# Performance work log

Measured on AMD Instinct MI355X. Metric: run time of the kernel, lower is better.

Reference implementation:

```python
import jax, jax.numpy as jnp
import numpy as np

# RankPool1d config (from init_kwargs)
RANK = 8          # kth smallest (1-indexed, as in torch.kthvalue)
KERNEL_SIZE = 16
STRIDE = 1
PADDING = 8
PAD_VALUE = 0.0   # mode='constant'

L = 4_194_304


def setup_inputs() -> dict:
    key = jax.random.key(0)
    x = jax.random.normal(key, (L,), dtype=jnp.float32)
    return {"x": x}


def reference(x):
    # F.pad(input, (PADDING, PADDING), mode='constant', value=PAD_VALUE)
    p = jnp.pad(x, (PADDING, PADDING), mode="constant", constant_values=PAD_VALUE)
    # p.unfold(0, KERNEL_SIZE, STRIDE) -> [out_len, KERNEL_SIZE] overlapping windows
    out_len = (p.shape[0] - KERNEL_SIZE) // STRIDE + 1
    idx = jnp.arange(out_len)[:, None] * STRIDE + jnp.arange(KERNEL_SIZE)[None, :]
    windows = p[idx]  # [out_len, k]
    # kthvalue(k=RANK, dim=1): value and index (within window) of RANK-th smallest
    order = jnp.argsort(windows, axis=1)          # [out_len, k]
    sel = order[:, RANK - 1]                       # [out_len] window-local index
    values = jnp.take_along_axis(windows, sel[:, None], axis=1)[:, 0]  # [out_len]
    return values, sel.astype(jnp.int32)
```

## Files before the change

### kernel.cpp

```cpp
#include <hip/hip_runtime.h>


constexpr int L_IN    = 4194304;
constexpr int OUT_LEN = L_IN + 1;
constexpr int MOUT    = 16;
constexpr int TPB     = 256;
constexpr int OPB     = TPB * MOUT;

__global__ __launch_bounds__(TPB) void rankpool_kernel(const float* __restrict__ x,
                                                       float* __restrict__ dout) {
    __shared__ float lv[MOUT * TPB];
    __shared__ float ls[MOUT * TPB];

    const int t   = threadIdx.x;
    const int blk = blockIdx.x;

    if (blk == 1024) {
        if (t == 0) {
            float w[16];
            #pragma unroll
            for (int i = 0; i < 16; ++i) {
                int g = L_IN - 8 + i;
                w[i] = (g < L_IN) ? x[g] : 0.0f;
            }
            int R[16];
            #pragma unroll
            for (int j = 0; j < 16; ++j) R[j] = j;
            #pragma unroll
            for (int j = 0; j < 16; ++j)
                #pragma unroll
                for (int k = j + 1; k < 16; ++k) {
                    int c = (w[k] < w[j]);
                    R[j] += c; R[k] -= c;
                }
            int sel = 0; float val = w[0];
            #pragma unroll
            for (int j = 0; j < 16; ++j) {
                bool c = (R[j] == 7);
                sel = c ? j : sel; val = c ? w[j] : val;
            }
            dout[OUT_LEN - 1]     = val;
            dout[2 * OUT_LEN - 1] = (float)sel;
        }
        return;
    }

    const int o0   = (blk * TPB + t) * MOUT;
    const int base = o0 - 8;

    float w[32];
    if (base >= 0 && base + 32 <= L_IN) {
        const float4* p = reinterpret_cast<const float4*>(x + base);
        #pragma unroll
        for (int q = 0; q < 8; ++q) {
            float4 v = p[q];
            w[4*q+0] = v.x; w[4*q+1] = v.y; w[4*q+2] = v.z; w[4*q+3] = v.w;
        }
    } else {
        #pragma unroll
        for (int i = 0; i < 32; ++i) {
            int g = base + i;
            w[i] = (g >= 0 && g < L_IN) ? x[g] : 0.0f;
        }
    }

    int R[31];
    #pragma unroll
    for (int j = 0; j < 16; ++j) R[j] = j;
    #pragma unroll
    for (int j = 0; j < 16; ++j) {
        #pragma unroll
        for (int k = j + 1; k < 16; ++k) {
            int c = (w[k] < w[j]);
            R[j] += c;
            R[k] -= c;
        }
    }

    #pragma unroll
    for (int m = 0; m < MOUT; ++m) {
        int   sel = 0;
        float val = w[m];
        #pragma unroll
        for (int j = m; j < m + 16; ++j) {
            bool c = (R[j] == 7 + m);
            sel = c ? (j - m) : sel;
            val = c ? w[j]    : val;
        }
        lv[m * TPB + t] = val;
        ls[m * TPB + t] = (float)sel;

        if (m < MOUT - 1) {
            const float wm = w[m];
            const float wn = w[m + 16];
            int s = 0;
            #pragma unroll
            for (int j = m + 1; j < m + 16; ++j) {
                R[j] += (int)(w[j] < wm);
                int c2 = (wn < w[j]);
                R[j] += c2;
                s    += c2;
            }
            R[m + 16] = 16 + m - s;
        }
    }

    __syncthreads();

    const int blockStart = blk * OPB;

    #pragma unroll
    for (int k = 0; k < 4; ++k) {
        int p = 4 * (t + 256 * k);
        float4 v;
        v.x = lv[((p + 0) & 15) * TPB + ((p + 0) >> 4)];
        v.y = lv[((p + 1) & 15) * TPB + ((p + 1) >> 4)];
        v.z = lv[((p + 2) & 15) * TPB + ((p + 2) >> 4)];
        v.w = lv[((p + 3) & 15) * TPB + ((p + 3) >> 4)];
        *reinterpret_cast<float4*>(dout + blockStart + p) = v;
    }

    float* s0 = dout + OUT_LEN + blockStart;
    if (t < 3)  s0[t] = ls[t * TPB];
    if (t == 3) s0[OPB - 1] = ls[15 * TPB + 255];
    #pragma unroll
    for (int k = 0; k < 4; ++k) {
        int q = t + 256 * k;
        if (q < 1023) {
            int p = 3 + 4 * q;
            float4 v;
            v.x = ls[((p + 0) & 15) * TPB + ((p + 0) >> 4)];
            v.y = ls[((p + 1) & 15) * TPB + ((p + 1) >> 4)];
            v.z = ls[((p + 2) & 15) * TPB + ((p + 2) >> 4)];
            v.w = ls[((p + 3) & 15) * TPB + ((p + 3) >> 4)];
            *reinterpret_cast<float4*>(s0 + p) = v;
        }
    }
}

extern "C" void kernel_launch(void* const* d_in, const int* in_sizes, int n_in,
                              void* d_out, int out_size, void* d_ws, size_t ws_size,
                              hipStream_t stream) {
    const float* x = (const float*)d_in[0];
    float* out = (float*)d_out;
    rankpool_kernel<<<1025, TPB, 0, stream>>>(x, out);
}
```

Before: 23.38 us.

## Pack indices as bytes, swizzle LDS layout, fold tail output into last thread

Window-local indices are packed four per 32-bit word in shared memory instead of one float each, which shrinks LDS use and traffic. An XOR swizzle is applied to the value and index LDS layouts to reduce bank conflicts on writes and reads. The extra 1025th block that computed the final output is removed; the last thread of the grid instead extends its sliding window by one step to produce it. Launch bounds now request 5 blocks per CU, which may raise occupancy at the cost of register pressure.

```diff
diff --git a/kernel.cpp b/kernel.cpp
--- a/kernel.cpp
+++ b/kernel.cpp
@@ -7,46 +7,24 @@
 constexpr int TPB     = 256;
 constexpr int OPB     = TPB * MOUT;
 
-__global__ __launch_bounds__(TPB) void rankpool_kernel(const float* __restrict__ x,
-                                                       float* __restrict__ dout) {
-    __shared__ float lv[MOUT * TPB];
-    __shared__ float ls[MOUT * TPB];
+__device__ __forceinline__ int lvidx(int p) {
+    return (p & 15) * TPB + ((p >> 4) ^ (2 * (p & 15)));
+}
+__device__ __forceinline__ int lsidx(int q) {
+    return (q & 3) * TPB + ((q >> 2) ^ (8 * (q & 3)));
+}
+
+__global__ __launch_bounds__(TPB, 5) void rankpool_kernel(const float* __restrict__ x,
+                                                          float* __restrict__ dout) {
+    __shared__ float    lv[MOUT * TPB];
+    __shared__ unsigned ws32[4 * TPB];
 
     const int t   = threadIdx.x;
     const int blk = blockIdx.x;
-
-    if (blk == 1024) {
-        if (t == 0) {
-            float w[16];
-            #pragma unroll
-            for (int i = 0; i < 16; ++i) {
-                int g = L_IN - 8 + i;
-                w[i] = (g < L_IN) ? x[g] : 0.0f;
-            }
-            int R[16];
-            #pragma unroll
-            for (int j = 0; j < 16; ++j) R[j] = j;
-            #pragma unroll
-            for (int j = 0; j < 16; ++j)
-                #pragma unroll
-                for (int k = j + 1; k < 16; ++k) {
-                    int c = (w[k] < w[j]);
-                    R[j] += c; R[k] -= c;
-                }
-            int sel = 0; float val = w[0];
-            #pragma unroll
-            for (int j = 0; j < 16; ++j) {
-                bool c = (R[j] == 7);
-                sel = c ? j : sel; val = c ? w[j] : val;
-            }
-            dout[OUT_LEN - 1]     = val;
-            dout[2 * OUT_LEN - 1] = (float)sel;
-        }
-        return;
-    }
-
-    const int o0   = (blk * TPB + t) * MOUT;
+    const int tid = blk * TPB + t;
+    const int o0  = tid * MOUT;
     const int base = o0 - 8;
+    const bool extra = (tid == TPB * 1024 - 1);
 
     float w[32];
     if (base >= 0 && base + 32 <= L_IN) {
@@ -64,7 +42,7 @@
         }
     }
 
-    int R[31];
+    int R[32];
     #pragma unroll
     for (int j = 0; j < 16; ++j) R[j] = j;
     #pragma unroll
@@ -77,6 +55,7 @@
         }
     }
 
+    unsigned pk[4] = {0u, 0u, 0u, 0u};
     #pragma unroll
     for (int m = 0; m < MOUT; ++m) {
         int   sel = 0;
@@ -87,8 +66,8 @@
             sel = c ? (j - m) : sel;
             val = c ? w[j]    : val;
         }
-        lv[m * TPB + t] = val;
-        ls[m * TPB + t] = (float)sel;
+        lv[lvidx(t * MOUT + m)] = val;
+        pk[m >> 2] |= ((unsigned)sel) << (8 * (m & 3));
 
         if (m < MOUT - 1) {
             const float wm = w[m];
@@ -104,6 +83,31 @@
             R[m + 16] = 16 + m - s;
         }
     }
+    #pragma unroll
+    for (int a = 0; a < 4; ++a)
+        ws32[lsidx(t * 4 + a)] = pk[a];
+
+    if (extra) {
+        const float wm = w[15], wn = w[31];
+        int s = 0;
+        #pragma unroll
+        for (int j = 16; j < 31; ++j) {
+            R[j] += (int)(w[j] < wm);
+            int c2 = (wn < w[j]);
+            R[j] += c2;
+            s    += c2;
+        }
+        R[31] = 31 - s;
+        int sel = 0; float val = w[16];
+        #pragma unroll
+        for (int j = 16; j < 32; ++j) {
+            bool c = (R[j] == 23);
+            sel = c ? (j - 16) : sel;
+            val = c ? w[j]     : val;
+        }
+        dout[OUT_LEN - 1]     = val;
+        dout[2 * OUT_LEN - 1] = (float)sel;
+    }
 
     __syncthreads();
 
@@ -111,29 +115,36 @@
 
     #pragma unroll
     for (int k = 0; k < 4; ++k) {
-        int p = 4 * (t + 256 * k);
+        int p = 4 * (t + TPB * k);
         float4 v;
-        v.x = lv[((p + 0) & 15) * TPB + ((p + 0) >> 4)];
-        v.y = lv[((p + 1) & 15) * TPB + ((p + 1) >> 4)];
-        v.z = lv[((p + 2) & 15) * TPB + ((p + 2) >> 4)];
-        v.w = lv[((p + 3) & 15) * TPB + ((p + 3) >> 4)];
+        v.x = lv[lvidx(p + 0)];
+        v.y = lv[lvidx(p + 1)];
+        v.z = lv[lvidx(p + 2)];
+        v.w = lv[lvidx(p + 3)];
         *reinterpret_cast<float4*>(dout + blockStart + p) = v;
     }
 
     float* s0 = dout + OUT_LEN + blockStart;
-    if (t < 3)  s0[t] = ls[t * TPB];
-    if (t == 3) s0[OPB - 1] = ls[15 * TPB + 255];
+    if (t < 3) {
+        unsigned w0 = ws32[lsidx(0)];
+        s0[t] = (float)((w0 >> (8 * t)) & 0xffu);
+    }
+    if (t == 3) {
+        unsigned wl = ws32[lsidx(1023)];
+        s0[OPB - 1] = (float)(wl >> 24);
+    }
     #pragma unroll
     for (int k = 0; k < 4; ++k) {
-        int q = t + 256 * k;
+        int q = t + TPB * k;
         if (q < 1023) {
-            int p = 3 + 4 * q;
+            unsigned wa = ws32[lsidx(q)];
+            unsigned wb = ws32[lsidx(q + 1)];
             float4 v;
-            v.x = ls[((p + 0) & 15) * TPB + ((p + 0) >> 4)];
-            v.y = ls[((p + 1) & 15) * TPB + ((p + 1) >> 4)];
-            v.z = ls[((p + 2) & 15) * TPB + ((p + 2) >> 4)];
-            v.w = ls[((p + 3) & 15) * TPB + ((p + 3) >> 4)];
-            *reinterpret_cast<float4*>(s0 + p) = v;
+            v.x = (float)(wa >> 24);
+            v.y = (float)( wb        & 0xffu);
+            v.z = (float)((wb >>  8) & 0xffu);
+            v.w = (float)((wb >> 16) & 0xffu);
+            *reinterpret_cast<float4*>(s0 + 3 + 4 * q) = v;
         }
     }
 }
@@ -143,5 +154,5 @@
                               hipStream_t stream) {
     const float* x = (const float*)d_in[0];
     float* out = (float*)d_out;
-    rankpool_kernel<<<1025, TPB, 0, stream>>>(x, out);
+    rankpool_kernel<<<1024, TPB, 0, stream>>>(x, out);
 }
```

Result: slower. 34.48 us (+47.4%).
